# Kernel tuning notes

Hardware: AMD Instinct MI355X
Metric: run time of the kernel (lower is better)

The kernel has to match this reference:

```python
import jax, jax.numpy as jnp
import numpy as np

N, D, F, C = 50000, 16, 128, 40  # nodes, fixed neighbor count, feat dim (hidden/2), classes


def _w(k, shape, fan_in):
    return jax.random.normal(k, shape, jnp.float32) / np.float32(np.sqrt(fan_in))


def setup_inputs() -> dict:
    key = jax.random.key(0)
    ks = jax.random.split(key, 8)
    z = lambda *s: jnp.zeros(s, jnp.float32)
    inp = {
        "x": jax.random.normal(ks[0], (N, F), jnp.float32),
        "edge_src": jax.random.randint(ks[1], (N, D), 0, N),  # dst is implicitly arange(N), sorted
        "W1": _w(ks[2], (F, F), F), "b1": z(F),
        "W2": _w(ks[3], (3 * F, F), F), "b2": z(3 * F),
        "W3": _w(ks[4], (F, 3 * F), 3 * F), "b3": z(F),
    }
    for i, (kb, oc) in (("1", (ks[5], F)), ("2", (ks[6], C))):
        pass  # placeholder (loop built below)
    for i, kb, oc in (("1", ks[5], F), ("2", ks[6], C)):
        kk = jax.random.split(kb, 5)
        inp["Wp" + i] = _w(kk[0], (F, F), F); inp["bp" + i] = z(F)
        inp["Wih" + i] = _w(kk[1], (4 * F, F), F)
        inp["Whh" + i] = _w(kk[2], (4 * F, F), F)
        inp["bih" + i] = z(4 * F); inp["bhh" + i] = z(4 * F)
        inp["Wl" + i] = _w(kk[3], (oc, F), F); inp["bl" + i] = z(oc)
        inp["Wr" + i] = _w(kk[4], (oc, F), F)
    return inp


def lstm_last(seq, Wih, Whh, bih, bhh):
    """seq: [N, T, F] -> final hidden state [N, H] (torch LSTM gate order i,f,g,o)."""
    Hh = Whh.shape[1]
    b = bih + bhh

    def step(carry, xt):
        h, c = carry
        g = xt @ Wih.T + h @ Whh.T + b
        i, f, gg, o = jnp.split(g, 4, axis=-1)
        c = jax.nn.sigmoid(f) * c + jax.nn.sigmoid(i) * jnp.tanh(gg)
        h = jax.nn.sigmoid(o) * jnp.tanh(c)
        return (h, c), None

    h0 = jnp.zeros((seq.shape[0], Hh), seq.dtype)
    (h, _), _ = jax.lax.scan(step, (h0, h0), jnp.swapaxes(seq, 0, 1))
    return h


def sage_conv_lstm(x, edge_src, Wp, bp, Wih, Whh, bih, bhh, Wl, bl, Wr):
    """PyG SAGEConv(aggr='lstm', project=True) with fixed per-node degree D."""
    xp = jax.nn.relu(x @ Wp.T + bp)           # project source features
    msgs = xp[edge_src]                        # [N, D, F] neighbor gather (sorted by dst)
    aggr = lstm_last(msgs, Wih, Whh, bih, bhh)  # LSTM over each neighborhood
    return aggr @ Wl.T + bl + x @ Wr.T         # lin_l(aggr) + lin_r(root)


def reference(x, edge_src, W1, b1, W2, b2, W3, b3,
              Wp1, bp1, Wih1, Whh1, bih1, bhh1, Wl1, bl1, Wr1,
              Wp2, bp2, Wih2, Whh2, bih2, bhh2, Wl2, bl2, Wr2):
    # Dead MLP branch: original forward computes it then overwrites h with conv1(x, ...)
    h = jax.nn.relu(x @ W1.T + b1)
    h = jax.nn.relu(h @ W2.T + b2)
    h = jax.nn.relu(h @ W3.T + b3)
    del h
    h = jax.nn.relu(sage_conv_lstm(x, edge_src, Wp1, bp1, Wih1, Whh1, bih1, bhh1, Wl1, bl1, Wr1))
    return sage_conv_lstm(h, edge_src, Wp2, bp2, Wih2, Whh2, bih2, bhh2, Wl2, bl2, Wr2)
```

## Files before the change

### kernel.cpp

```cpp
#include <hip/hip_runtime.h>
#include <hip/hip_bf16.h>


typedef __hip_bfloat16 bf16;
typedef __attribute__((ext_vector_type(8))) short short8;
typedef __attribute__((ext_vector_type(4))) short short4v;
typedef __attribute__((ext_vector_type(4))) float floatx4;
typedef __attribute__((ext_vector_type(4))) float float4v;

#define LOG2E 1.4426950408889634f
#define TWOL  2.8853900817779268f

__device__ __forceinline__ float bf2f(bf16 v) { return __bfloat162float(v); }
__device__ __forceinline__ bf16  f2bf(float v) { return __float2bfloat16(v); }
__device__ __forceinline__ float bfs2f(short s) {
    union { float f; unsigned u; } v; v.u = ((unsigned)(unsigned short)s) << 16; return v.f;
}
__device__ __forceinline__ short f2bfs(float v) {
    bf16 b = __float2bfloat16(v); return *(short*)&b;
}

__device__ __forceinline__ float ex2(float x) {
#if __has_builtin(__builtin_amdgcn_exp2f)
    return __builtin_amdgcn_exp2f(x);
#else
    return exp2f(x);
#endif
}

__device__ __forceinline__ float cell(float i_, float f_, float g_, float o_, float& c) {
    float ei = ex2(-i_), ef = ex2(-f_), eg = ex2(g_), eo = ex2(-o_);
    float A = (1.f + ei) * (eg + 1.f);
    float B = 1.f + ef;
    float cn = fmaf(c, A, fmaf(eg, TWOL, -TWOL) * B) * __builtin_amdgcn_rcpf(A * B);
    c = cn;
    float ec = ex2(cn);
    return (ec - 1.f) * __builtin_amdgcn_rcpf((ec + 1.f) * (1.f + eo));
}

__device__ __forceinline__ int ydecode(int p) {
    int pw = (p >> 6) & 7, pq = (p >> 4) & 3, pg = (p >> 2) & 3, pr = p & 3;
    return pg * 128 + pw * 16 + pq * 4 + pr;
}

__device__ __forceinline__ short8 load_x8(const void* X, bool isf32, size_t row, int off) {
    if (isf32) {
        const float* p = (const float*)X + row * 128 + off;
        float4v a = *(const float4v*)p, b = *(const float4v*)(p + 4);
        short8 r;
#pragma unroll
        for (int j = 0; j < 4; j++) { r[j] = f2bfs(a[j]); r[4 + j] = f2bfs(b[j]); }
        return r;
    }
    return *(const short8*)((const bf16*)X + row * 128 + off);
}

__device__ __forceinline__ void dma1(const bf16* gp, void* lp) {
    __builtin_amdgcn_global_load_lds(
        (const __attribute__((address_space(1))) void*)gp,
        (__attribute__((address_space(3))) void*)lp, 16, 0, 0);
}

__device__ __forceinline__ void dma2(const bf16* gp, void* lp0, void* lp1) {
    dma1(gp, lp0);
    dma1(gp + 32, lp1);
}

struct Cvt { const void* src; const void* src2; bf16* dst; int n; int mode; };
struct CvtAll { Cvt t[16]; };

__global__ void convert_inputs(CvtAll ca, const unsigned short* __restrict__ xb,
                               int* __restrict__ flag) {
    __shared__ int sflag;
    {
        int cnt = 0;
        for (int i = threadIdx.x; i < 1024; i += blockDim.x) {
            int e = (xb[i] >> 7) & 0xFF;
            cnt += (e >= 0xC8);
        }
        if (threadIdx.x == 0) sflag = 0;
        __syncthreads();
        if (cnt) atomicAdd(&sflag, cnt);
        __syncthreads();
    }
    const bool isf32 = (sflag >= 16);
    if (blockIdx.x == 0 && threadIdx.x == 0) *flag = isf32 ? 1 : 0;

    const int stride = gridDim.x * blockDim.x;
    const int tid0 = blockIdx.x * blockDim.x + threadIdx.x;
#pragma unroll 1
    for (int k = 0; k < 16; k++) {
        const int n = ca.t[k].n, mode = ca.t[k].mode;
        if (mode == 3) {
            const float* a32 = (const float*)ca.t[k].src;
            const float* b32 = (const float*)ca.t[k].src2;
            const short* a16 = (const short*)ca.t[k].src;
            const short* b16 = (const short*)ca.t[k].src2;
            float* df = (float*)ca.t[k].dst;
            for (int i = tid0; i < n; i += stride) {
                int yd = ydecode(i);
                float va = isf32 ? a32[yd] : bfs2f(a16[yd]);
                float vb = isf32 ? b32[yd] : bfs2f(b16[yd]);
                float m = ((((unsigned)i >> 2) & 3) == 2) ? TWOL : LOG2E;
                df[i] = (va + vb) * m;
            }
            continue;
        }
        const int n8 = n >> 3;
        bf16* d = ca.t[k].dst;
        for (int i = tid0; i < n8; i += stride) {
            int si = i;
            float m = 1.f;
            bool scaled = false;
            if (mode == 1) {
                m = ((((unsigned)i >> 11) & 3) == 2) ? TWOL : LOG2E; scaled = true;
            } else if (mode == 2) {
                int row = i >> 4;
                si = ydecode(row) * 16 + (i & 15);
                m = ((((unsigned)row >> 2) & 3) == 2) ? TWOL : LOG2E; scaled = true;
            }
            short8 ov;
            if (isf32) {
                const float4v* sp = (const float4v*)ca.t[k].src;
                float4v a = sp[2 * si], b = sp[2 * si + 1];
#pragma unroll
                for (int j = 0; j < 4; j++) {
                    ov[j]     = f2bfs(a[j] * m);
                    ov[4 + j] = f2bfs(b[j] * m);
                }
            } else {
                short8 sv = ((const short8*)ca.t[k].src)[si];
                if (scaled) {
#pragma unroll
                    for (int j = 0; j < 8; j++) ov[j] = f2bfs(bfs2f(sv[j]) * m);
                } else ov = sv;
            }
            ((short8*)d)[i] = ov;
        }
        if (mode == 0)
            for (int i = (n8 << 3) + tid0; i < n; i += stride) {
                float v = isf32 ? ((const float*)ca.t[k].src)[i]
                                : bfs2f(((const short*)ca.t[k].src)[i]);
                d[i] = f2bf(v);
            }
    }
}

__global__ __launch_bounds__(256, 3) void fused_xp_y(
    const void* __restrict__ Xraw, const int* __restrict__ flag,
    const bf16* __restrict__ Wp, const bf16* __restrict__ bp,
    const bf16* __restrict__ Wihp, const float* __restrict__ bsum,
    bf16* __restrict__ Yout, int N)
{
    __shared__ bf16 T[64][136];
    const int tid = threadIdx.x;
    const int w = tid >> 6, l = tid & 63, q = l >> 4, lid = l & 15;
    const int rowbase = blockIdx.x * 64;
    const bool isf32 = (*flag != 0);

    int arow = rowbase + w * 16 + lid;
    if (arow >= N) arow = N - 1;

    {
        floatx4 acc[8];
        float bvv[8];
#pragma unroll
        for (int ct = 0; ct < 8; ct++) {
            acc[ct] = (floatx4)(0.f);
            bvv[ct] = bf2f(bp[lid * 8 + ct]);
        }
#pragma unroll
        for (int kh = 0; kh < 2; kh++) {
            short8 bfrag[8][2];
#pragma unroll
            for (int ct = 0; ct < 8; ct++)
#pragma unroll
                for (int k2 = 0; k2 < 2; k2++)
                    bfrag[ct][k2] = *(const short8*)(Wp + (size_t)(lid * 8 + ct) * 128 + (kh * 2 + k2) * 32 + q * 8);
#pragma unroll
            for (int k2 = 0; k2 < 2; k2++) {
                short8 af = load_x8(Xraw, isf32, (size_t)arow, (kh * 2 + k2) * 32 + q * 8);
#pragma unroll
                for (int ct = 0; ct < 8; ct++)
                    acc[ct] = __builtin_amdgcn_mfma_f32_16x16x32_bf16(af, bfrag[ct][k2], acc[ct], 0, 0, 0);
            }
        }
#pragma unroll
        for (int r = 0; r < 4; r++) {
            short8 ov;
#pragma unroll
            for (int ct = 0; ct < 8; ct++)
                ov[ct] = f2bfs(fmaxf(acc[ct][r] + bvv[ct], 0.f));
            *(short8*)&T[w * 16 + q * 4 + r][lid * 8] = ov;
        }
    }
    __syncthreads();

#pragma unroll 1
    for (int hf = 0; hf < 2; hf++) {
        short8 wfr[4][4];
        float bv2[4];
#pragma unroll
        for (int ct = 0; ct < 4; ct++) {
            int pos = w * 128 + lid * 8 + hf * 4 + ct;
            bv2[ct] = bsum[pos];
#pragma unroll
            for (int kt = 0; kt < 4; kt++)
                wfr[ct][kt] = *(const short8*)(Wihp + (size_t)pos * 128 + kt * 32 + q * 8);
        }
#pragma unroll 1
        for (int rt = 0; rt < 4; rt++) {
            floatx4 a2[4];
#pragma unroll
            for (int ct = 0; ct < 4; ct++) a2[ct] = (floatx4)(0.f);
#pragma unroll
            for (int kt = 0; kt < 4; kt++) {
                short8 af = *(const short8*)&T[rt * 16 + lid][kt * 32 + q * 8];
#pragma unroll
                for (int ct = 0; ct < 4; ct++)
                    a2[ct] = __builtin_amdgcn_mfma_f32_16x16x32_bf16(af, wfr[ct][kt], a2[ct], 0, 0, 0);
            }
#pragma unroll
            for (int r = 0; r < 4; r++) {
                int row = rowbase + rt * 16 + q * 4 + r;
                if (row < N) {
                    short4v ov;
#pragma unroll
                    for (int ct = 0; ct < 4; ct++)
                        ov[ct] = f2bfs(a2[ct][r] + bv2[ct]);
                    *(short4v*)(Yout + (size_t)row * 512 + w * 128 + lid * 8 + hf * 4) = ov;
                }
            }
        }
    }
}

__global__ __launch_bounds__(256, 3) void fused_lin_xp_y(
    const bf16* __restrict__ aggr, const bf16* __restrict__ Wl, const bf16* __restrict__ bl,
    const void* __restrict__ Xraw, const int* __restrict__ flag,
    const bf16* __restrict__ Wr,
    bf16* __restrict__ h1out,
    const bf16* __restrict__ Wp2, const bf16* __restrict__ bp2,
    const bf16* __restrict__ Wihp2, const float* __restrict__ bsum2,
    bf16* __restrict__ Yout, int N)
{
    __shared__ bf16 T1[64][136];
    __shared__ bf16 T2[64][136];
    const int tid = threadIdx.x;
    const int w = tid >> 6, l = tid & 63, q = l >> 4, lid = l & 15;
    const int rowbase = blockIdx.x * 64;
    const bool isf32 = (*flag != 0);

    int arow = rowbase + w * 16 + lid;
    if (arow >= N) arow = N - 1;

    {
        floatx4 acc[8];
        float bvv[8];
#pragma unroll
        for (int ct = 0; ct < 8; ct++) {
            acc[ct] = (floatx4)(0.f);
            bvv[ct] = bf2f(bl[lid * 8 + ct]);
        }
#pragma unroll
        for (int kh = 0; kh < 2; kh++) {
            short8 bfrag[8][2];
#pragma unroll
            for (int ct = 0; ct < 8; ct++)
#pragma unroll
                for (int k2 = 0; k2 < 2; k2++)
                    bfrag[ct][k2] = *(const short8*)(Wl + (size_t)(lid * 8 + ct) * 128 + (kh * 2 + k2) * 32 + q * 8);
#pragma unroll
            for (int k2 = 0; k2 < 2; k2++) {
                short8 af = *(const short8*)(aggr + (size_t)arow * 128 + (kh * 2 + k2) * 32 + q * 8);
#pragma unroll
                for (int ct = 0; ct < 8; ct++)
                    acc[ct] = __builtin_amdgcn_mfma_f32_16x16x32_bf16(af, bfrag[ct][k2], acc[ct], 0, 0, 0);
            }
        }
#pragma unroll
        for (int kh = 0; kh < 2; kh++) {
            short8 bfrag[8][2];
#pragma unroll
            for (int ct = 0; ct < 8; ct++)
#pragma unroll
                for (int k2 = 0; k2 < 2; k2++)
                    bfrag[ct][k2] = *(const short8*)(Wr + (size_t)(lid * 8 + ct) * 128 + (kh * 2 + k2) * 32 + q * 8);
#pragma unroll
            for (int k2 = 0; k2 < 2; k2++) {
                short8 af = load_x8(Xraw, isf32, (size_t)arow, (kh * 2 + k2) * 32 + q * 8);
#pragma unroll
                for (int ct = 0; ct < 8; ct++)
                    acc[ct] = __builtin_amdgcn_mfma_f32_16x16x32_bf16(af, bfrag[ct][k2], acc[ct], 0, 0, 0);
            }
        }
#pragma unroll
        for (int r = 0; r < 4; r++) {
            short8 ov;
#pragma unroll
            for (int ct = 0; ct < 8; ct++)
                ov[ct] = f2bfs(fmaxf(acc[ct][r] + bvv[ct], 0.f));
            int rl = w * 16 + q * 4 + r;
            *(short8*)&T1[rl][lid * 8] = ov;
            int row = rowbase + rl;
            if (row < N) *(short8*)(h1out + (size_t)row * 128 + lid * 8) = ov;
        }
    }
    __syncthreads();

    {
        floatx4 acc[8];
        float bvv[8];
#pragma unroll
        for (int ct = 0; ct < 8; ct++) {
            acc[ct] = (floatx4)(0.f);
            bvv[ct] = bf2f(bp2[lid * 8 + ct]);
        }
#pragma unroll
        for (int kh = 0; kh < 2; kh++) {
            short8 bfrag[8][2];
#pragma unroll
            for (int ct = 0; ct < 8; ct++)
#pragma unroll
                for (int k2 = 0; k2 < 2; k2++)
                    bfrag[ct][k2] = *(const short8*)(Wp2 + (size_t)(lid * 8 + ct) * 128 + (kh * 2 + k2) * 32 + q * 8);
#pragma unroll
            for (int k2 = 0; k2 < 2; k2++) {
                short8 af = *(const short8*)&T1[w * 16 + lid][(kh * 2 + k2) * 32 + q * 8];
#pragma unroll
                for (int ct = 0; ct < 8; ct++)
                    acc[ct] = __builtin_amdgcn_mfma_f32_16x16x32_bf16(af, bfrag[ct][k2], acc[ct], 0, 0, 0);
            }
        }
#pragma unroll
        for (int r = 0; r < 4; r++) {
            short8 ov;
#pragma unroll
            for (int ct = 0; ct < 8; ct++)
                ov[ct] = f2bfs(fmaxf(acc[ct][r] + bvv[ct], 0.f));
            *(short8*)&T2[w * 16 + q * 4 + r][lid * 8] = ov;
        }
    }
    __syncthreads();

#pragma unroll 1
    for (int hf = 0; hf < 2; hf++) {
        short8 wfr[4][4];
        float bv2[4];
#pragma unroll
        for (int ct = 0; ct < 4; ct++) {
            int pos = w * 128 + lid * 8 + hf * 4 + ct;
            bv2[ct] = bsum2[pos];
#pragma unroll
            for (int kt = 0; kt < 4; kt++)
                wfr[ct][kt] = *(const short8*)(Wihp2 + (size_t)pos * 128 + kt * 32 + q * 8);
        }
#pragma unroll 1
        for (int rt = 0; rt < 4; rt++) {
            floatx4 a2[4];
#pragma unroll
            for (int ct = 0; ct < 4; ct++) a2[ct] = (floatx4)(0.f);
#pragma unroll
            for (int kt = 0; kt < 4; kt++) {
                short8 af = *(const short8*)&T2[rt * 16 + lid][kt * 32 + q * 8];
#pragma unroll
                for (int ct = 0; ct < 4; ct++)
                    a2[ct] = __builtin_amdgcn_mfma_f32_16x16x32_bf16(af, wfr[ct][kt], a2[ct], 0, 0, 0);
            }
#pragma unroll
            for (int r = 0; r < 4; r++) {
                int row = rowbase + rt * 16 + q * 4 + r;
                if (row < N) {
                    short4v ov;
#pragma unroll
                    for (int ct = 0; ct < 4; ct++)
                        ov[ct] = f2bfs(a2[ct][r] + bv2[ct]);
                    *(short4v*)(Yout + (size_t)row * 512 + w * 128 + lid * 8 + hf * 4) = ov;
                }
            }
        }
    }
}

template <int EPI>
__global__ __launch_bounds__(512, 4) void lstm_aggr(
    const bf16* __restrict__ Y,
    const int* __restrict__ esrc,
    const bf16* __restrict__ Whh,
    bf16* __restrict__ aggr,
    int N,
    const bf16* __restrict__ Wl2, const bf16* __restrict__ bl2,
    const bf16* __restrict__ Wr2, const bf16* __restrict__ h1,
    void* __restrict__ outp, const int* __restrict__ oflag)
{
    __shared__ alignas(16) short stage[2][8][1024];
    __shared__ alignas(16) bf16 hb[2][16][136];
    __shared__ int srcl[16][16];

    const int tid = threadIdx.x;
    const int w = tid >> 6, l = tid & 63, q = l >> 4, lid = l & 15;
    const int nodebase = blockIdx.x * 16;

    if (tid < 256) {
        int node = tid >> 4, t = tid & 15;
        srcl[t][node] = esrc[(size_t)(nodebase + node) * 16 + t];
    }

    short8 wf[4][4];
#pragma unroll
    for (int g = 0; g < 4; g++) {
        int gc = g * 128 + 16 * w + lid;
#pragma unroll
        for (int kt = 0; kt < 4; kt++)
            wf[g][kt] = *(const short8*)(Whh + (size_t)gc * 128 + kt * 32 + q * 8);
    }

    float c[4];
#pragma unroll
    for (int r = 0; r < 4; r++) c[r] = 0.f;

    const int laneoff = w * 64 + q * 8;

    __syncthreads();

    {
        int s0 = srcl[0][lid];
        dma2(Y + (size_t)s0 * 512 + laneoff, &stage[0][w][0], &stage[0][w][512]);
        int s1 = srcl[1][lid];
        dma2(Y + (size_t)s1 * 512 + laneoff, &stage[1][w][0], &stage[1][w][512]);
    }

#pragma unroll 2
    for (int t = 0; t < 16; t++) {
        const int cb = t & 1;

        if (t == 15) asm volatile("s_waitcnt vmcnt(0)" ::: "memory");
        else         asm volatile("s_waitcnt vmcnt(2)" ::: "memory");

        if (EPI == 1 && t == 15 && w < 4) {
            int row = w * 4 + q;
            const bf16* gp = h1 + (size_t)(nodebase + row) * 128 + (lid ^ (row & 7)) * 8;
            dma1(gp, (char*)&stage[0][0][0] + w * 1024);
        }

        int snext = (t < 14) ? srcl[t + 2][lid] : 0;

        floatx4 acc[4];
        {
            const short* wbuf = &stage[cb][w][0];
            short8 y0 = *(const short8*)&wbuf[q * 256 + lid * 8];
            short8 y1 = *(const short8*)&wbuf[q * 256 + 128 + lid * 8];
#pragma unroll
            for (int g = 0; g < 2; g++)
#pragma unroll
                for (int r = 0; r < 4; r++) {
                    acc[g][r]     = bfs2f(y0[g * 4 + r]);
                    acc[2 + g][r] = bfs2f(y1[g * 4 + r]);
                }
        }

        if (t) {
#pragma unroll
            for (int kt = 0; kt < 4; kt++) {
                short8 bh = *(const short8*)&hb[cb][lid][kt * 32 + q * 8];
#pragma unroll
                for (int g = 0; g < 4; g++)
                    acc[g] = __builtin_amdgcn_mfma_f32_16x16x32_bf16(wf[g][kt], bh, acc[g], 0, 0, 0);
            }
        }

        {
            short4v hv;
#pragma unroll
            for (int r = 0; r < 4; r++)
                hv[r] = f2bfs(cell(acc[0][r], acc[1][r], acc[2][r], acc[3][r], c[r]));
            if (t < 15) *(short4v*)&hb[cb ^ 1][lid][16 * w + 4 * q] = hv;
            else if (EPI == 0)
                *(short4v*)(aggr + (size_t)(nodebase + lid) * 128 + 16 * w + 4 * q) = hv;
            else
                *(short4v*)&hb[0][lid][16 * w + 4 * q] = hv;
        }

        if (t < 15) {
            asm volatile("s_waitcnt lgkmcnt(0)" ::: "memory");
            if (t < 14)
                dma2(Y + (size_t)snext * 512 + laneoff, &stage[cb][w][0], &stage[cb][w][512]);
            __builtin_amdgcn_s_barrier();
        }
    }

    if constexpr (EPI == 1) {
        asm volatile("s_waitcnt vmcnt(0)" ::: "memory");
        short8 blf[4], brf[4];
        int j = w * 16 + lid;
        int jc = j < 40 ? j : 39;
        if (w < 3) {
#pragma unroll
            for (int kt = 0; kt < 4; kt++) {
                blf[kt] = *(const short8*)(Wl2 + (size_t)jc * 128 + kt * 32 + q * 8);
                brf[kt] = *(const short8*)(Wr2 + (size_t)jc * 128 + kt * 32 + q * 8);
            }
        }
        asm volatile("s_waitcnt lgkmcnt(0)" ::: "memory");
        __builtin_amdgcn_s_barrier();
        if (w < 3) {
            const short* xs = &stage[0][0][0];
            floatx4 o = (floatx4)(0.f);
#pragma unroll
            for (int kt = 0; kt < 4; kt++) {
                short8 ah = *(const short8*)&hb[0][lid][kt * 32 + q * 8];
                o = __builtin_amdgcn_mfma_f32_16x16x32_bf16(ah, blf[kt], o, 0, 0, 0);
            }
#pragma unroll
            for (int kt = 0; kt < 4; kt++) {
                short8 a1 = *(const short8*)&xs[lid * 128 + (((kt * 4 + q) ^ (lid & 7)) << 3)];
                o = __builtin_amdgcn_mfma_f32_16x16x32_bf16(a1, brf[kt], o, 0, 0, 0);
            }
            float bv = bf2f(bl2[jc]);
            bool of32 = (*oflag != 0);
            if (j < 40) {
#pragma unroll
                for (int r = 0; r < 4; r++) {
                    int node = nodebase + q * 4 + r;
                    float v = o[r] + bv;
                    size_t idx = (size_t)node * 40 + j;
                    if (of32) ((float*)outp)[idx] = v;
                    else      ((bf16*)outp)[idx]  = f2bf(v);
                }
            }
        }
    }
}

extern "C" void kernel_launch(void* const* d_in, const int* in_sizes, int n_in,
                              void* d_out, int out_size, void* d_ws, size_t ws_size,
                              hipStream_t stream)
{
    const int N = 50000;
    const int* es = (const int*)d_in[1];
    char* ws = (char*)d_ws;

    struct Ent { int di; int di2; int mode; };
    Ent ents[16] = {
        {8,  -1, 0}, {9,  -1, 0},
        {10, -1, 2}, {11, -1, 1},
        {12, 13, 3},
        {14, -1, 0}, {15, -1, 0}, {16, -1, 0},
        {17, -1, 0}, {18, -1, 0},
        {19, -1, 2}, {20, -1, 1},
        {21, 22, 3},
        {23, -1, 0}, {24, -1, 0}, {25, -1, 0},
    };
    bf16* conv[16];
    size_t off = 0;
    CvtAll ca;
    for (int k = 0; k < 16; k++) {
        conv[k] = (bf16*)ws + off;
        int n = in_sizes[ents[k].di];
        ca.t[k].src  = d_in[ents[k].di];
        ca.t[k].src2 = ents[k].di2 >= 0 ? d_in[ents[k].di2] : nullptr;
        ca.t[k].dst  = conv[k];
        ca.t[k].n    = n;
        ca.t[k].mode = ents[k].mode;
        size_t elems = (ents[k].mode == 3) ? (size_t)n * 2 : (size_t)n;
        off += (elems + 63) & ~(size_t)63;
    }
    int* flag  = (int*)(ws + ((size_t)15 << 20));
    bf16* aggr = (bf16*)(ws + ((size_t)16 << 20));
    bf16* Y    = (bf16*)(ws + ((size_t)30 << 20));
    bf16* h1   = (bf16*)(ws + ((size_t)84 << 20));

    const void* xraw = d_in[0];
    const bf16 *Wp1  = conv[0],  *bp1 = conv[1];
    const bf16 *Wihp1 = conv[2], *Whh1 = conv[3];
    const float *bsum1 = (const float*)conv[4];
    const bf16 *Wl1 = conv[5], *bl1 = conv[6], *Wr1 = conv[7];
    const bf16 *Wp2 = conv[8], *bp2 = conv[9];
    const bf16 *Wihp2 = conv[10], *Whh2 = conv[11];
    const float *bsum2 = (const float*)conv[12];
    const bf16 *Wl2 = conv[13], *bl2 = conv[14], *Wr2 = conv[15];

    dim3 blk(256);
    const int gx = (N + 63) / 64;
    const int gl = N / 16;

    convert_inputs<<<dim3(128), blk, 0, stream>>>(
        ca, (const unsigned short*)d_in[0], flag);

    fused_xp_y<<<dim3(gx), blk, 0, stream>>>(xraw, flag, Wp1, bp1, Wihp1, bsum1, Y, N);
    lstm_aggr<0><<<dim3(gl), dim3(512), 0, stream>>>(
        Y, es, Whh1, aggr, N, nullptr, nullptr, nullptr, nullptr, nullptr, nullptr);

    fused_lin_xp_y<<<dim3(gx), blk, 0, stream>>>(
        aggr, Wl1, bl1, xraw, flag, Wr1, h1, Wp2, bp2, Wihp2, bsum2, Y, N);

    lstm_aggr<1><<<dim3(gl), dim3(512), 0, stream>>>(
        Y, es, Whh2, nullptr, N, Wl2, bl2, Wr2, h1, d_out, flag);
}
```

Baseline: 579.3 us.

## Interleave two node groups per LSTM aggregation block with triple-buffered staging

Each lstm_aggr block now processes 32 nodes as two independent 16-node groups whose LSTM recurrences are interleaved step by step. A three-slot rotating stage buffer lets the gather for one group's next step overlap the other group's MFMA and cell work, hiding the dependent recurrence latency and the global gather latency. The block count is halved and shared memory and register use grow, which may lower occupancy. The epilogue is adjusted to handle both groups and a possibly partial last block.

```diff
diff --git a/kernel.cpp b/kernel.cpp
--- a/kernel.cpp
+++ b/kernel.cpp
@@ -393,17 +393,22 @@
     const bf16* __restrict__ Wr2, const bf16* __restrict__ h1,
     void* __restrict__ outp, const int* __restrict__ oflag)
 {
-    __shared__ alignas(16) short stage[2][8][1024];
-    __shared__ alignas(16) bf16 hb[2][16][136];
-    __shared__ int srcl[16][16];
+    __shared__ alignas(16) short stage[3][8][1024];
+    __shared__ alignas(16) bf16 hbA[2][16][136];
+    __shared__ alignas(16) bf16 hbB[2][16][136];
+    __shared__ int srcl[16][32];
 
     const int tid = threadIdx.x;
     const int w = tid >> 6, l = tid & 63, q = l >> 4, lid = l & 15;
-    const int nodebase = blockIdx.x * 16;
-
-    if (tid < 256) {
-        int node = tid >> 4, t = tid & 15;
-        srcl[t][node] = esrc[(size_t)(nodebase + node) * 16 + t];
+    const int nodebase = blockIdx.x * 32;
+    const int nb2 = nodebase + 16;
+    const bool hasB = nb2 < N;
+
+    {
+        int node = tid & 31, t = tid >> 5;
+        int row = nodebase + node;
+        if (row >= N) row = N - 1;
+        srcl[t][node] = esrc[(size_t)row * 16 + t];
     }
 
     short8 wf[4][4];
@@ -415,39 +420,36 @@
             wf[g][kt] = *(const short8*)(Whh + (size_t)gc * 128 + kt * 32 + q * 8);
     }
 
-    float c[4];
-#pragma unroll
-    for (int r = 0; r < 4; r++) c[r] = 0.f;
-
-    const int laneoff = w * 64 + q * 8;
+    float cA[4], cB[4];
+#pragma unroll
+    for (int r = 0; r < 4; r++) { cA[r] = 0.f; cB[r] = 0.f; }
+
+    short* const sbase = &stage[0][0][0];
+    const int wb1k = w * 1024;
+    int oA = wb1k;
+    int oB = 8192 + wb1k;
+    const int K3 = 24576 + 3 * wb1k;
+    const int lo = w * 64 + q * 8;
 
     __syncthreads();
 
     {
-        int s0 = srcl[0][lid];
-        dma2(Y + (size_t)s0 * 512 + laneoff, &stage[0][w][0], &stage[0][w][512]);
-        int s1 = srcl[1][lid];
-        dma2(Y + (size_t)s1 * 512 + laneoff, &stage[1][w][0], &stage[1][w][512]);
-    }
-
-#pragma unroll 2
+        dma2(Y + (size_t)srcl[0][lid] * 512 + lo,      sbase + oA, sbase + oA + 512);
+        dma2(Y + (size_t)srcl[0][16 + lid] * 512 + lo, sbase + oB, sbase + oB + 512);
+        int oC = K3 - oA - oB;
+        dma2(Y + (size_t)srcl[1][lid] * 512 + lo,      sbase + oC, sbase + oC + 512);
+    }
+
+#pragma unroll
     for (int t = 0; t < 16; t++) {
         const int cb = t & 1;
 
-        if (t == 15) asm volatile("s_waitcnt vmcnt(0)" ::: "memory");
-        else         asm volatile("s_waitcnt vmcnt(2)" ::: "memory");
-
-        if (EPI == 1 && t == 15 && w < 4) {
-            int row = w * 4 + q;
-            const bf16* gp = h1 + (size_t)(nodebase + row) * 128 + (lid ^ (row & 7)) * 8;
-            dma1(gp, (char*)&stage[0][0][0] + w * 1024);
-        }
-
-        int snext = (t < 14) ? srcl[t + 2][lid] : 0;
+        if (t == 15) asm volatile("s_waitcnt vmcnt(2)" ::: "memory");
+        else         asm volatile("s_waitcnt vmcnt(4)" ::: "memory");
 
         floatx4 acc[4];
         {
-            const short* wbuf = &stage[cb][w][0];
+            const short* wbuf = sbase + oA;
             short8 y0 = *(const short8*)&wbuf[q * 256 + lid * 8];
             short8 y1 = *(const short8*)&wbuf[q * 256 + 128 + lid * 8];
 #pragma unroll
@@ -458,43 +460,90 @@
                     acc[2 + g][r] = bfs2f(y1[g * 4 + r]);
                 }
         }
-
         if (t) {
 #pragma unroll
             for (int kt = 0; kt < 4; kt++) {
-                short8 bh = *(const short8*)&hb[cb][lid][kt * 32 + q * 8];
+                short8 bh = *(const short8*)&hbA[cb][lid][kt * 32 + q * 8];
 #pragma unroll
                 for (int g = 0; g < 4; g++)
                     acc[g] = __builtin_amdgcn_mfma_f32_16x16x32_bf16(wf[g][kt], bh, acc[g], 0, 0, 0);
             }
         }
-
         {
-            short4v hv;
+            short4v hvA;
 #pragma unroll
             for (int r = 0; r < 4; r++)
-                hv[r] = f2bfs(cell(acc[0][r], acc[1][r], acc[2][r], acc[3][r], c[r]));
-            if (t < 15) *(short4v*)&hb[cb ^ 1][lid][16 * w + 4 * q] = hv;
-            else if (EPI == 0)
-                *(short4v*)(aggr + (size_t)(nodebase + lid) * 128 + 16 * w + 4 * q) = hv;
-            else
-                *(short4v*)&hb[0][lid][16 * w + 4 * q] = hv;
+                hvA[r] = f2bfs(cell(acc[0][r], acc[1][r], acc[2][r], acc[3][r], cA[r]));
+            if (t < 15)        *(short4v*)&hbA[cb ^ 1][lid][16 * w + 4 * q] = hvA;
+            else if (EPI == 0) *(short4v*)(aggr + (size_t)(nodebase + lid) * 128 + 16 * w + 4 * q) = hvA;
+            else               *(short4v*)&hbA[0][lid][16 * w + 4 * q] = hvA;
+        }
+
+        if (t == 15) asm volatile("s_waitcnt vmcnt(0)" ::: "memory");
+        else         asm volatile("s_waitcnt vmcnt(2)" ::: "memory");
+
+        if (EPI == 1 && t == 15) {
+            int r = w * 4 + q;
+            int node = nodebase + r;
+            if (node >= N) node = N - 1;
+            dma1(h1 + (size_t)node * 128 + (lid ^ (r & 7)) * 8,
+                 (char*)&stage[2][0][0] + w * 1024);
+        }
+
+        {
+            const short* wbuf = sbase + oB;
+            short8 y0 = *(const short8*)&wbuf[q * 256 + lid * 8];
+            short8 y1 = *(const short8*)&wbuf[q * 256 + 128 + lid * 8];
+#pragma unroll
+            for (int g = 0; g < 2; g++)
+#pragma unroll
+                for (int r = 0; r < 4; r++) {
+                    acc[g][r]     = bfs2f(y0[g * 4 + r]);
+                    acc[2 + g][r] = bfs2f(y1[g * 4 + r]);
+                }
+        }
+        if (t) {
+#pragma unroll
+            for (int kt = 0; kt < 4; kt++) {
+                short8 bh = *(const short8*)&hbB[cb][lid][kt * 32 + q * 8];
+#pragma unroll
+                for (int g = 0; g < 4; g++)
+                    acc[g] = __builtin_amdgcn_mfma_f32_16x16x32_bf16(wf[g][kt], bh, acc[g], 0, 0, 0);
+            }
+        }
+        {
+            short4v hvB;
+#pragma unroll
+            for (int r = 0; r < 4; r++)
+                hvB[r] = f2bfs(cell(acc[0][r], acc[1][r], acc[2][r], acc[3][r], cB[r]));
+            if (t < 15)        *(short4v*)&hbB[cb ^ 1][lid][16 * w + 4 * q] = hvB;
+            else if (EPI == 0) { if (hasB)
+                *(short4v*)(aggr + (size_t)(nb2 + lid) * 128 + 16 * w + 4 * q) = hvB; }
+            else               *(short4v*)&hbB[0][lid][16 * w + 4 * q] = hvB;
         }
 
         if (t < 15) {
             asm volatile("s_waitcnt lgkmcnt(0)" ::: "memory");
+            dma2(Y + (size_t)srcl[t + 1][16 + lid] * 512 + lo,
+                 sbase + oA, sbase + oA + 512);
             if (t < 14)
-                dma2(Y + (size_t)snext * 512 + laneoff, &stage[cb][w][0], &stage[cb][w][512]);
+                dma2(Y + (size_t)srcl[t + 2][lid] * 512 + lo,
+                     sbase + oB, sbase + oB + 512);
             __builtin_amdgcn_s_barrier();
+            int oC = K3 - oA - oB;
+            oB = oA;
+            oA = oC;
         }
     }
 
     if constexpr (EPI == 1) {
         asm volatile("s_waitcnt vmcnt(0)" ::: "memory");
+        const int grp = w >> 2;
+        const int we = w & 3;
+        int j = we * 16 + lid;
+        int jc = j < 40 ? j : 39;
         short8 blf[4], brf[4];
-        int j = w * 16 + lid;
-        int jc = j < 40 ? j : 39;
-        if (w < 3) {
+        if (we < 3) {
 #pragma unroll
             for (int kt = 0; kt < 4; kt++) {
                 blf[kt] = *(const short8*)(Wl2 + (size_t)jc * 128 + kt * 32 + q * 8);
@@ -503,17 +552,19 @@
         }
         asm volatile("s_waitcnt lgkmcnt(0)" ::: "memory");
         __builtin_amdgcn_s_barrier();
-        if (w < 3) {
-            const short* xs = &stage[0][0][0];
+        if (we < 3 && (grp == 0 || hasB)) {
+            const short* xs = &stage[2][0][0];
+            const bf16 (*hbp)[136] = grp ? hbB[0] : hbA[0];
+            const int rbase = grp * 16;
             floatx4 o = (floatx4)(0.f);
 #pragma unroll
             for (int kt = 0; kt < 4; kt++) {
-                short8 ah = *(const short8*)&hb[0][lid][kt * 32 + q * 8];
+                short8 ah = *(const short8*)&hbp[lid][kt * 32 + q * 8];
                 o = __builtin_amdgcn_mfma_f32_16x16x32_bf16(ah, blf[kt], o, 0, 0, 0);
             }
 #pragma unroll
             for (int kt = 0; kt < 4; kt++) {
-                short8 a1 = *(const short8*)&xs[lid * 128 + (((kt * 4 + q) ^ (lid & 7)) << 3)];
+                short8 a1 = *(const short8*)&xs[(rbase + lid) * 128 + (((kt * 4 + q) ^ (lid & 7)) << 3)];
                 o = __builtin_amdgcn_mfma_f32_16x16x32_bf16(a1, brf[kt], o, 0, 0, 0);
             }
             float bv = bf2f(bl2[jc]);
@@ -521,7 +572,7 @@
             if (j < 40) {
 #pragma unroll
                 for (int r = 0; r < 4; r++) {
-                    int node = nodebase + q * 4 + r;
+                    int node = nodebase + rbase + q * 4 + r;
                     float v = o[r] + bv;
                     size_t idx = (size_t)node * 40 + j;
                     if (of32) ((float*)outp)[idx] = v;
@@ -582,7 +633,7 @@
 
     dim3 blk(256);
     const int gx = (N + 63) / 64;
-    const int gl = N / 16;
+    const int gl = (N + 31) / 32;
 
     convert_inputs<<<dim3(128), blk, 0, stream>>>(
         ca, (const unsigned short*)d_in[0], flag);
```

New measurement: 575.5 us. About the same (-0.7%).
